# Performance work log

Hardware: AMD Instinct MI355X
Metric: run time of the kernel (lower is better)

## Reference

```python
import jax, jax.numpy as jnp
import numpy as np

EPSILON = 5.0
B, D, C = 262144, 512, 1000


def setup_inputs() -> dict:
    key = jax.random.key(0)
    k1, k2, k3 = jax.random.split(key, 3)
    features = jax.random.normal(k1, (B, D), dtype=jnp.float32)
    means = jax.random.normal(k2, (C, D), dtype=jnp.float32)
    labels = jax.random.randint(k3, (B,), 0, C, dtype=jnp.int64)
    return {"features": features, "means": means, "labels": labels}


def reference(features, means, labels):
    # Gather per-sample class mean: [B, D]
    gathered = means[labels]
    diff = features - gathered
    # Per-sample L2 distance, then hinge clamp(epsilon - dist, min=0), mean over batch
    dist = jnp.sqrt(jnp.sum(diff * diff, axis=-1))  # [B]
    loss = jnp.mean(jnp.maximum(EPSILON - dist, 0.0))
    return loss
```

## Files before the change

kernel.cpp:

```cpp
#include <hip/hip_runtime.h>

#define EPSILON 5.0f

constexpr int BLOCKS  = 2048;
constexpr int THREADS = 256;

__global__ __launch_bounds__(THREADS) void ncl_partial_kernel(
    const float* __restrict__ features,
    const float* __restrict__ means,
    const int* __restrict__ labels,
    float* __restrict__ partials,
    int B)
{
    const int lane = threadIdx.x & 63;
    const int sub  = lane & 15;
    const int g    = lane >> 4;
    const int globalWave = blockIdx.x * (THREADS >> 6) + (threadIdx.x >> 6);
    const int totalWaves = gridDim.x * (THREADS >> 6);
    const int nQuads = (B + 3) >> 2;

    float wsum = 0.0f;

    int q   = globalWave;
    int row = q * 4 + g;
    int cls = (q < nQuads && row < B) ? labels[row] : 0;

    for (; q < nQuads; q += totalWaves) {
        row = q * 4 + g;
        const bool valid = (row < B);

        const int nq   = q + totalWaves;
        const int nrow = nq * 4 + g;
        const int ncls = (nq < nQuads && nrow < B) ? labels[nrow] : 0;

        float acc = 0.0f;
        if (valid) {
            const float4* f = reinterpret_cast<const float4*>(features) + (size_t)row * 128;
            const float4* m = reinterpret_cast<const float4*>(means)    + (size_t)cls * 128;
            #pragma unroll
            for (int k = 0; k < 8; ++k) {
                const float4 fv = f[sub + 16 * k];
                const float4 mv = m[sub + 16 * k];
                const float dx = fv.x - mv.x;
                const float dy = fv.y - mv.y;
                const float dz = fv.z - mv.z;
                const float dw = fv.w - mv.w;
                acc = fmaf(dx, dx, fmaf(dy, dy, fmaf(dz, dz, fmaf(dw, dw, acc))));
            }
        }

        #pragma unroll
        for (int off = 8; off > 0; off >>= 1)
            acc += __shfl_xor(acc, off, 64);

        if (sub == 0 && valid)
            wsum += fmaxf(EPSILON - sqrtf(acc), 0.0f);

        cls = ncls;
    }

    #pragma unroll
    for (int off = 32; off > 0; off >>= 1)
        wsum += __shfl_xor(wsum, off, 64);

    __shared__ float s[THREADS >> 6];
    const int wv = threadIdx.x >> 6;
    if (lane == 0) s[wv] = wsum;
    __syncthreads();
    if (threadIdx.x == 0) {
        float t = 0.0f;
        #pragma unroll
        for (int i = 0; i < (THREADS >> 6); ++i) t += s[i];
        partials[blockIdx.x] = t;
    }
}

__global__ __launch_bounds__(THREADS) void ncl_final_kernel(
    const float* __restrict__ partials,
    int n,
    float* __restrict__ out,
    float invB)
{
    float t = 0.0f;
    for (int i = threadIdx.x; i < n; i += THREADS) t += partials[i];

    #pragma unroll
    for (int off = 32; off > 0; off >>= 1)
        t += __shfl_xor(t, off, 64);

    __shared__ float s[THREADS >> 6];
    const int lane = threadIdx.x & 63;
    const int wv   = threadIdx.x >> 6;
    if (lane == 0) s[wv] = t;
    __syncthreads();
    if (threadIdx.x == 0) {
        float acc = 0.0f;
        #pragma unroll
        for (int i = 0; i < (THREADS >> 6); ++i) acc += s[i];
        out[0] = acc * invB;
    }
}

extern "C" void kernel_launch(void* const* d_in, const int* in_sizes, int n_in,
                              void* d_out, int out_size, void* d_ws, size_t ws_size,
                              hipStream_t stream) {
    const float* features = (const float*)d_in[0];
    const float* means    = (const float*)d_in[1];
    const int*   labels   = (const int*)d_in[2];
    float* out = (float*)d_out;

    const int B = in_sizes[2];
    float* partials = (float*)d_ws;

    ncl_partial_kernel<<<BLOCKS, THREADS, 0, stream>>>(features, means, labels,
                                                       partials, B);
    ncl_final_kernel<<<1, THREADS, 0, stream>>>(partials, BLOCKS, out,
                                                1.0f / (float)B);
}
```

Baseline: 114.3 us.

## Process one row per wave with register double-buffered nontemporal feature loads

Each wave now handles a whole row (64 lanes × 2 float4) instead of four rows per wave with 16 lanes each. Next-row features and means are loaded into registers before the current row is computed, and labels are prefetched two rows ahead. Feature loads use nontemporal hints so the streaming data does not pollute cache. The intent is more memory-level parallelism per wave and less cache thrashing, at the cost of a full 64-wide shuffle reduction per row and fewer loads in flight per row.

```diff
diff --git a/kernel.cpp b/kernel.cpp
--- a/kernel.cpp
+++ b/kernel.cpp
@@ -4,6 +4,8 @@
 
 constexpr int BLOCKS  = 2048;
 constexpr int THREADS = 256;
+
+typedef float fx4 __attribute__((ext_vector_type(4)));
 
 __global__ __launch_bounds__(THREADS) void ncl_partial_kernel(
     const float* __restrict__ features,
@@ -13,55 +15,65 @@
     int B)
 {
     const int lane = threadIdx.x & 63;
-    const int sub  = lane & 15;
-    const int g    = lane >> 4;
     const int globalWave = blockIdx.x * (THREADS >> 6) + (threadIdx.x >> 6);
     const int totalWaves = gridDim.x * (THREADS >> 6);
-    const int nQuads = (B + 3) >> 2;
+
+    const fx4* __restrict__ F = reinterpret_cast<const fx4*>(features);
+    const fx4* __restrict__ M = reinterpret_cast<const fx4*>(means);
 
     float wsum = 0.0f;
 
-    int q   = globalWave;
-    int row = q * 4 + g;
-    int cls = (q < nQuads && row < B) ? labels[row] : 0;
+    int row = globalWave;
+    int cls0 = (row < B) ? labels[row] : 0;
+    {
+        const int r1 = row + totalWaves;
+        int cls1 = (r1 < B) ? labels[r1] : 0;
 
-    for (; q < nQuads; q += totalWaves) {
-        row = q * 4 + g;
-        const bool valid = (row < B);
-
-        const int nq   = q + totalWaves;
-        const int nrow = nq * 4 + g;
-        const int ncls = (nq < nQuads && nrow < B) ? labels[nrow] : 0;
-
-        float acc = 0.0f;
-        if (valid) {
-            const float4* f = reinterpret_cast<const float4*>(features) + (size_t)row * 128;
-            const float4* m = reinterpret_cast<const float4*>(means)    + (size_t)cls * 128;
-            #pragma unroll
-            for (int k = 0; k < 8; ++k) {
-                const float4 fv = f[sub + 16 * k];
-                const float4 mv = m[sub + 16 * k];
-                const float dx = fv.x - mv.x;
-                const float dy = fv.y - mv.y;
-                const float dz = fv.z - mv.z;
-                const float dw = fv.w - mv.w;
-                acc = fmaf(dx, dx, fmaf(dy, dy, fmaf(dz, dz, fmaf(dw, dw, acc))));
-            }
+        fx4 f0 = {0,0,0,0}, f1 = {0,0,0,0}, m0 = {0,0,0,0}, m1 = {0,0,0,0};
+        if (row < B) {
+            const fx4* f = F + (size_t)row  * 128;
+            const fx4* m = M + (size_t)cls0 * 128;
+            f0 = __builtin_nontemporal_load(f + lane);
+            f1 = __builtin_nontemporal_load(f + lane + 64);
+            m0 = m[lane];
+            m1 = m[lane + 64];
         }
 
-        #pragma unroll
-        for (int off = 8; off > 0; off >>= 1)
-            acc += __shfl_xor(acc, off, 64);
+        while (row < B) {
+            const int nrow = row + totalWaves;
 
-        if (sub == 0 && valid)
-            wsum += fmaxf(EPSILON - sqrtf(acc), 0.0f);
+            fx4 nf0 = {0,0,0,0}, nf1 = {0,0,0,0}, nm0 = {0,0,0,0}, nm1 = {0,0,0,0};
+            if (nrow < B) {
+                const fx4* f = F + (size_t)nrow * 128;
+                const fx4* m = M + (size_t)cls1 * 128;
+                nf0 = __builtin_nontemporal_load(f + lane);
+                nf1 = __builtin_nontemporal_load(f + lane + 64);
+                nm0 = m[lane];
+                nm1 = m[lane + 64];
+            }
+            const int r2   = row + 2 * totalWaves;
+            const int cls2 = (r2 < B) ? labels[r2] : 0;
 
-        cls = ncls;
+            fx4 d0 = f0 - m0;
+            fx4 d1 = f1 - m1;
+            float ax = d0.x * d0.x, ay = d0.y * d0.y,
+                  az = d0.z * d0.z, aw = d0.w * d0.w;
+            ax = fmaf(d1.x, d1.x, ax); ay = fmaf(d1.y, d1.y, ay);
+            az = fmaf(d1.z, d1.z, az); aw = fmaf(d1.w, d1.w, aw);
+            float acc = (ax + ay) + (az + aw);
+
+            #pragma unroll
+            for (int off = 32; off > 0; off >>= 1)
+                acc += __shfl_xor(acc, off, 64);
+
+            if (lane == 0)
+                wsum += fmaxf(EPSILON - sqrtf(acc), 0.0f);
+
+            f0 = nf0; f1 = nf1; m0 = nm0; m1 = nm1;
+            cls1 = cls2;
+            row  = nrow;
+        }
     }
-
-    #pragma unroll
-    for (int off = 32; off > 0; off >>= 1)
-        wsum += __shfl_xor(wsum, off, 64);
 
     __shared__ float s[THREADS >> 6];
     const int wv = threadIdx.x >> 6;
```

Measured after the change: 102.4 us. -10.4%, faster.

## Software-pipeline feature loads with register double-buffering and nontemporal loads

Applied to the files above, without the earlier changes.

Restructures the per-wave loop so each full wave processes four rows, with every lane holding two float4s per row. The next quad's features and labels are prefetched into registers while the current quad is computed. Feature loads use nontemporal hints so the streamed data does not pollute cache, and the reduction becomes a full 64-lane butterfly per row. This adds register pressure and drops tail handling when B is not a multiple of 4.

```diff
diff --git a/kernel.cpp b/kernel.cpp
--- a/kernel.cpp
+++ b/kernel.cpp
@@ -4,6 +4,8 @@
 
 constexpr int BLOCKS  = 2048;
 constexpr int THREADS = 256;
+
+typedef float fx4 __attribute__((ext_vector_type(4)));
 
 __global__ __launch_bounds__(THREADS) void ncl_partial_kernel(
     const float* __restrict__ features,
@@ -13,55 +15,107 @@
     int B)
 {
     const int lane = threadIdx.x & 63;
-    const int sub  = lane & 15;
-    const int g    = lane >> 4;
-    const int globalWave = blockIdx.x * (THREADS >> 6) + (threadIdx.x >> 6);
-    const int totalWaves = gridDim.x * (THREADS >> 6);
-    const int nQuads = (B + 3) >> 2;
+    const int gw = blockIdx.x * (THREADS >> 6) + (threadIdx.x >> 6);
+    const int T = gridDim.x * (THREADS >> 6);
+    const int nQ = B >> 2;
+
+    const fx4* __restrict__ F = reinterpret_cast<const fx4*>(features);
+    const fx4* __restrict__ M = reinterpret_cast<const fx4*>(means);
 
     float wsum = 0.0f;
 
-    int q   = globalWave;
-    int row = q * 4 + g;
-    int cls = (q < nQuads && row < B) ? labels[row] : 0;
+    int q = gw;
 
-    for (; q < nQuads; q += totalWaves) {
-        row = q * 4 + g;
-        const bool valid = (row < B);
+    int c0 = 0, c1 = 0, c2 = 0, c3 = 0;
+    if (q < nQ) {
+        const int base = 4 * q;
+        c0 = labels[base];     c1 = labels[base + 1];
+        c2 = labels[base + 2]; c3 = labels[base + 3];
+    }
 
-        const int nq   = q + totalWaves;
-        const int nrow = nq * 4 + g;
-        const int ncls = (nq < nQuads && nrow < B) ? labels[nrow] : 0;
+    fx4 f00{0,0,0,0}, f01{0,0,0,0}, f10{0,0,0,0}, f11{0,0,0,0};
+    fx4 f20{0,0,0,0}, f21{0,0,0,0}, f30{0,0,0,0}, f31{0,0,0,0};
+    if (q < nQ) {
+        const fx4* f0 = F + (size_t)(4 * q)     * 128;
+        const fx4* f1 = F + (size_t)(4 * q + 1) * 128;
+        const fx4* f2 = F + (size_t)(4 * q + 2) * 128;
+        const fx4* f3 = F + (size_t)(4 * q + 3) * 128;
+        f00 = __builtin_nontemporal_load(f0 + lane);
+        f01 = __builtin_nontemporal_load(f0 + lane + 64);
+        f10 = __builtin_nontemporal_load(f1 + lane);
+        f11 = __builtin_nontemporal_load(f1 + lane + 64);
+        f20 = __builtin_nontemporal_load(f2 + lane);
+        f21 = __builtin_nontemporal_load(f2 + lane + 64);
+        f30 = __builtin_nontemporal_load(f3 + lane);
+        f31 = __builtin_nontemporal_load(f3 + lane + 64);
+    }
 
-        float acc = 0.0f;
-        if (valid) {
-            const float4* f = reinterpret_cast<const float4*>(features) + (size_t)row * 128;
-            const float4* m = reinterpret_cast<const float4*>(means)    + (size_t)cls * 128;
-            #pragma unroll
-            for (int k = 0; k < 8; ++k) {
-                const float4 fv = f[sub + 16 * k];
-                const float4 mv = m[sub + 16 * k];
-                const float dx = fv.x - mv.x;
-                const float dy = fv.y - mv.y;
-                const float dz = fv.z - mv.z;
-                const float dw = fv.w - mv.w;
-                acc = fmaf(dx, dx, fmaf(dy, dy, fmaf(dz, dz, fmaf(dw, dw, acc))));
-            }
+    while (q < nQ) {
+        const int nq = q + T;
+
+        fx4 g00{0,0,0,0}, g01{0,0,0,0}, g10{0,0,0,0}, g11{0,0,0,0};
+        fx4 g20{0,0,0,0}, g21{0,0,0,0}, g30{0,0,0,0}, g31{0,0,0,0};
+        if (nq < nQ) {
+            const fx4* f0 = F + (size_t)(4 * nq)     * 128;
+            const fx4* f1 = F + (size_t)(4 * nq + 1) * 128;
+            const fx4* f2 = F + (size_t)(4 * nq + 2) * 128;
+            const fx4* f3 = F + (size_t)(4 * nq + 3) * 128;
+            g00 = __builtin_nontemporal_load(f0 + lane);
+            g01 = __builtin_nontemporal_load(f0 + lane + 64);
+            g10 = __builtin_nontemporal_load(f1 + lane);
+            g11 = __builtin_nontemporal_load(f1 + lane + 64);
+            g20 = __builtin_nontemporal_load(f2 + lane);
+            g21 = __builtin_nontemporal_load(f2 + lane + 64);
+            g30 = __builtin_nontemporal_load(f3 + lane);
+            g31 = __builtin_nontemporal_load(f3 + lane + 64);
         }
 
+        const fx4* m0 = M + (size_t)c0 * 128;
+        const fx4* m1 = M + (size_t)c1 * 128;
+        const fx4* m2 = M + (size_t)c2 * 128;
+        const fx4* m3 = M + (size_t)c3 * 128;
+        const fx4 m00 = m0[lane], m01 = m0[lane + 64];
+        const fx4 m10 = m1[lane], m11 = m1[lane + 64];
+        const fx4 m20 = m2[lane], m21 = m2[lane + 64];
+        const fx4 m30 = m3[lane], m31 = m3[lane + 64];
+
+        int d0 = 0, d1 = 0, d2 = 0, d3 = 0;
+        if (nq < nQ) {
+            const int base = 4 * nq;
+            d0 = labels[base];     d1 = labels[base + 1];
+            d2 = labels[base + 2]; d3 = labels[base + 3];
+        }
+
+        fx4 e, v0, v1, v2, v3;
+        e = f00 - m00; v0 = e * e;  e = f01 - m01; v0 = e * e + v0;
+        e = f10 - m10; v1 = e * e;  e = f11 - m11; v1 = e * e + v1;
+        e = f20 - m20; v2 = e * e;  e = f21 - m21; v2 = e * e + v2;
+        e = f30 - m30; v3 = e * e;  e = f31 - m31; v3 = e * e + v3;
+        float a0 = (v0.x + v0.y) + (v0.z + v0.w);
+        float a1 = (v1.x + v1.y) + (v1.z + v1.w);
+        float a2 = (v2.x + v2.y) + (v2.z + v2.w);
+        float a3 = (v3.x + v3.y) + (v3.z + v3.w);
+
         #pragma unroll
-        for (int off = 8; off > 0; off >>= 1)
-            acc += __shfl_xor(acc, off, 64);
+        for (int off = 32; off > 0; off >>= 1) {
+            a0 += __shfl_xor(a0, off, 64);
+            a1 += __shfl_xor(a1, off, 64);
+            a2 += __shfl_xor(a2, off, 64);
+            a3 += __shfl_xor(a3, off, 64);
+        }
 
-        if (sub == 0 && valid)
-            wsum += fmaxf(EPSILON - sqrtf(acc), 0.0f);
+        if (lane == 0) {
+            wsum += fmaxf(EPSILON - sqrtf(a0), 0.0f)
+                  + fmaxf(EPSILON - sqrtf(a1), 0.0f)
+                  + fmaxf(EPSILON - sqrtf(a2), 0.0f)
+                  + fmaxf(EPSILON - sqrtf(a3), 0.0f);
+        }
 
-        cls = ncls;
+        f00 = g00; f01 = g01; f10 = g10; f11 = g11;
+        f20 = g20; f21 = g21; f30 = g30; f31 = g31;
+        c0 = d0; c1 = d1; c2 = d2; c3 = d3;
+        q = nq;
     }
-
-    #pragma unroll
-    for (int off = 32; off > 0; off >>= 1)
-        wsum += __shfl_xor(wsum, off, 64);
 
     __shared__ float s[THREADS >> 6];
     const int wv = threadIdx.x >> 6;
```

New measurement: 96.43 us, median of 2. -15.7%, faster.
